# Kernel tuning notes

Hardware: AMD Instinct MI355X
Metric: run time of the kernel (lower is better)

## Reference

```python
import jax, jax.numpy as jnp
import numpy as np
import math

N_BITS = 3
N_EMBD = 2048
N_HEAD = 16
B, T = 1, 2048


def fake_quant_act(x, bits=N_BITS):
    # Brevitas Int8ActPerTensorFloat at 3 bits: signed, non-narrow range [-4, 3]
    qmin, qmax = -(2 ** (bits - 1)), 2 ** (bits - 1) - 1
    s = jax.lax.stop_gradient(jnp.max(jnp.abs(x))) / (2 ** (bits - 1))
    q = jnp.clip(jnp.round(x / s), qmin, qmax) * s
    return x + jax.lax.stop_gradient(q - x)  # STE


def fake_quant_weight(w, bits=N_BITS):
    # Int8WeightPerTensorFloat, narrow_range=True at 3 bits: range [-3, 3]
    qmax = 2 ** (bits - 1) - 1
    s = jax.lax.stop_gradient(jnp.max(jnp.abs(w))) / qmax
    q = jnp.clip(jnp.round(w / s), -qmax, qmax) * s
    return w + jax.lax.stop_gradient(q - w)  # STE


def setup_inputs() -> dict:
    key = jax.random.key(0)
    ks = jax.random.split(key, 7)
    W_STD = 0.02  # GPT-style init keeps exp(att) in range (own_softmax has no max-subtract)
    x = jax.random.normal(ks[0], (B, T, N_EMBD), dtype=jnp.float32)
    W1 = jax.random.normal(ks[1], (N_EMBD, N_EMBD), dtype=jnp.float32) * W_STD
    W2 = jax.random.normal(ks[2], (N_EMBD, N_EMBD), dtype=jnp.float32) * W_STD
    W3 = jax.random.normal(ks[3], (N_EMBD, N_EMBD), dtype=jnp.float32) * W_STD
    b1 = jax.random.normal(ks[4], (N_EMBD,), dtype=jnp.float32) * W_STD
    b2 = jax.random.normal(ks[5], (N_EMBD,), dtype=jnp.float32) * W_STD
    b3 = jax.random.normal(ks[6], (N_EMBD,), dtype=jnp.float32) * W_STD
    return {"x": x, "W1": W1, "b1": b1, "W2": W2, "b2": b2, "W3": W3, "b3": b3}


def reference(x, W1, b1, W2, b2, W3, b3):
    hs = N_EMBD // N_HEAD
    xq = fake_quant_act(x)  # quant_inp
    q = xq @ fake_quant_weight(W1).T + b1  # c_attn1
    k = xq @ fake_quant_weight(W2).T + b2  # c_attn2
    v = xq @ fake_quant_weight(W3).T + b3  # c_attn3
    # [B,T,C] -> [B,nh,T,hs]
    q = q.reshape(B, T, N_HEAD, hs).transpose(0, 2, 1, 3)
    k = k.reshape(B, T, N_HEAD, hs).transpose(0, 2, 1, 3)
    v = v.reshape(B, T, N_HEAD, hs).transpose(0, 2, 1, 3)
    att = jnp.einsum("bhqd,bhkd->bhqk", q, k) * (1.0 / math.sqrt(hs))
    # own_softmax: exp normalized over dim=1 == the HEAD axis (faithful to source; no mask)
    e = jnp.exp(att)
    att = e / jnp.sum(e, axis=1, keepdims=True)
    # attn_dropout p=0 -> identity; c_proj never applied in forward
    y = jnp.einsum("bhqk,bhkd->bhqd", att, v)  # [B,nh,T,hs]
    return y
```

## Files before the change

### kernel.cpp

```cpp
#include <hip/hip_runtime.h>
#include <hip/hip_bf16.h>

typedef short bf16x8 __attribute__((ext_vector_type(8)));
typedef float f32x4 __attribute__((ext_vector_type(4)));
typedef unsigned short u16;

constexpr int TOKS = 2048;
constexpr int EMB  = 2048;
constexpr int NH   = 16;
constexpr int HS   = 128;
constexpr float RSQ = 0.08838834764831845f;

constexpr size_t OFF_SCAL = 0;
constexpr size_t OFF_QX   = 1024;
constexpr size_t SZ_MAT   = (size_t)TOKS * EMB * 2;
constexpr size_t OFF_QW   = OFF_QX + SZ_MAT;
constexpr size_t OFF_Q    = OFF_QW + 3 * SZ_MAT;
constexpr size_t OFF_K    = OFF_Q + SZ_MAT;
constexpr size_t OFF_V    = OFF_K + SZ_MAT;
constexpr size_t OFF_VT   = OFF_V + SZ_MAT;
constexpr size_t OFF_DEN  = OFF_VT + SZ_MAT;

#define VMCNT(n) asm volatile("s_waitcnt vmcnt(" #n ")" ::: "memory")
#define LGKM0()  asm volatile("s_waitcnt lgkmcnt(0)" ::: "memory")
#define BAR()    do { asm volatile("" ::: "memory"); __builtin_amdgcn_s_barrier(); asm volatile("" ::: "memory"); } while (0)

__device__ __forceinline__ u16 f2b(float f) {
  unsigned u = __float_as_uint(f);
  unsigned r = (u + 0x7fffu + ((u >> 16) & 1u)) >> 16;
  return (u16)r;
}

__device__ __forceinline__ unsigned cvtpk(float a, float b) {
  unsigned r;
  asm("v_cvt_pk_bf16_f32 %0, %1, %2" : "=v"(r) : "v"(a), "v"(b));
  return r;
}

__device__ __forceinline__ void gload16(const void* g, void* l) {
  __builtin_amdgcn_global_load_lds(
      (const __attribute__((address_space(1))) unsigned int*)g,
      (__attribute__((address_space(3))) unsigned int*)l, 16, 0, 0);
}

__global__ void k_init(int* scal) {
  if (threadIdx.x < 4) scal[threadIdx.x] = 0;
}

__global__ void k_absmax(const float* __restrict__ x, const float* __restrict__ w1,
                         const float* __restrict__ w2, const float* __restrict__ w3,
                         int* scal) {
  const float* src = (blockIdx.y == 0) ? x : (blockIdx.y == 1) ? w1 : (blockIdx.y == 2) ? w2 : w3;
  const float4* s4 = (const float4*)src;
  int idx = blockIdx.x * 256 + threadIdx.x;
  float m = 0.f;
  for (int i = 0; i < 16; ++i) {
    float4 v = s4[idx + i * 65536];
    m = fmaxf(m, fmaxf(fmaxf(fabsf(v.x), fabsf(v.y)), fmaxf(fabsf(v.z), fabsf(v.w))));
  }
  for (int o = 32; o; o >>= 1) m = fmaxf(m, __shfl_down(m, o));
  __shared__ float red[4];
  if ((threadIdx.x & 63) == 0) red[threadIdx.x >> 6] = m;
  __syncthreads();
  if (threadIdx.x == 0) {
    m = fmaxf(fmaxf(red[0], red[1]), fmaxf(red[2], red[3]));
    atomicMax(&scal[blockIdx.y], __float_as_int(m));
  }
}

__global__ void k_quant(const float* __restrict__ x, const float* __restrict__ w1,
                        const float* __restrict__ w2, const float* __restrict__ w3,
                        u16* qx, u16* qw, const int* scal) {
  int a = blockIdx.y;
  const float* src = (a == 0) ? x : (a == 1) ? w1 : (a == 2) ? w2 : w3;
  u16* dst = (a == 0) ? qx : qw + (size_t)(a - 1) * TOKS * EMB;
  float mx = __int_as_float(scal[a]);
  float s = (a == 0) ? mx * 0.25f : mx / 3.0f;
  float lo = (a == 0) ? -4.f : -3.f;
  const float hi = 3.f;
  int idx = blockIdx.x * 256 + threadIdx.x;
  for (int i = 0; i < 16; ++i) {
    int j = idx + i * 65536;
    float4 v = ((const float4*)src)[j];
    ushort4 o;
    o.x = f2b(fminf(fmaxf(rintf(v.x / s), lo), hi));
    o.y = f2b(fminf(fmaxf(rintf(v.y / s), lo), hi));
    o.z = f2b(fminf(fmaxf(rintf(v.z / s), lo), hi));
    o.w = f2b(fminf(fmaxf(rintf(v.w / s), lo), hi));
    ((ushort4*)dst)[j] = o;
  }
}

__global__ __launch_bounds__(256, 3) void k_gemm(const u16* __restrict__ qx, const u16* __restrict__ qw,
    const float* __restrict__ b1, const float* __restrict__ b2, const float* __restrict__ b3,
    const int* __restrict__ scal, u16* qo, u16* ko, u16* vo) {
  int z = blockIdx.z;
  const u16* W = qw + (size_t)z * TOKS * EMB;
  const float* bias = (z == 0) ? b1 : (z == 1) ? b2 : b3;
  u16* out = (z == 0) ? qo : (z == 1) ? ko : vo;
  float sx = __int_as_float(scal[0]) * 0.25f;
  float sw = __int_as_float(scal[1 + z]) / 3.0f;
  float alpha = sx * sw;
  float extra = (z == 0) ? RSQ : 1.0f;
  int t0 = blockIdx.y * 128, o0 = blockIdx.x * 128;
  __shared__ __align__(16) u16 As[128 * 64];
  __shared__ __align__(16) u16 Bs[128 * 64];
  int tid = threadIdx.x, lane = tid & 63, wid = tid >> 6;
  int mh = (wid >> 1) * 64, nh = (wid & 1) * 64;
  f32x4 acc[4][4] = {};
  const char* Ab = (const char*)qx;
  const char* Bb = (const char*)W;
  for (int kk = 0; kk < 32; ++kk) {
#pragma unroll
    for (int p = 0; p < 4; ++p) {
      int L = p * 4096 + tid * 16;
      int r = L >> 7;
      int s = ((L >> 4) & 7) ^ (r & 7);
      gload16(Ab + (size_t)(t0 + r) * 4096 + kk * 128 + s * 16,
              (char*)As + p * 4096 + wid * 1024);
      gload16(Bb + (size_t)(o0 + r) * 4096 + kk * 128 + s * 16,
              (char*)Bs + p * 4096 + wid * 1024);
    }
    __syncthreads();
#pragma unroll
    for (int ks = 0; ks < 2; ++ks) {
      bf16x8 af[4], bfr[4];
#pragma unroll
      for (int m = 0; m < 4; ++m) {
        int row = mh + m * 16 + (lane & 15);
        int sl = (ks * 4 + (lane >> 4)) ^ (row & 7);
        af[m] = *(const bf16x8*)((const char*)As + row * 128 + sl * 16);
      }
#pragma unroll
      for (int n = 0; n < 4; ++n) {
        int row = nh + n * 16 + (lane & 15);
        int sl = (ks * 4 + (lane >> 4)) ^ (row & 7);
        bfr[n] = *(const bf16x8*)((const char*)Bs + row * 128 + sl * 16);
      }
#pragma unroll
      for (int m = 0; m < 4; ++m)
#pragma unroll
        for (int n = 0; n < 4; ++n)
          acc[m][n] = __builtin_amdgcn_mfma_f32_16x16x32_bf16(af[m], bfr[n], acc[m][n], 0, 0, 0);
    }
    __syncthreads();
  }
#pragma unroll
  for (int m = 0; m < 4; ++m)
#pragma unroll
    for (int n = 0; n < 4; ++n) {
      int ocol = o0 + nh + n * 16 + (lane & 15);
      float bb = bias[ocol];
#pragma unroll
      for (int r = 0; r < 4; ++r) {
        int trow = t0 + mh + m * 16 + (lane >> 4) * 4 + r;
        float v = (acc[m][n][r] * alpha + bb) * extra;
        out[(size_t)trow * EMB + ocol] = f2b(v);
      }
    }
}

__global__ void k_transpose(const u16* __restrict__ v, u16* vt) {
  int h = blockIdx.z, d0 = blockIdx.y * 64, t0 = blockIdx.x * 64;
  __shared__ u16 tile[64][65];
  int tid = threadIdx.x;
  for (int i = 0; i < 16; ++i) {
    int idx = i * 256 + tid, r = idx >> 6, c = idx & 63;
    tile[r][c] = v[(size_t)(t0 + r) * EMB + h * HS + d0 + c];
  }
  __syncthreads();
  for (int i = 0; i < 16; ++i) {
    int idx = i * 256 + tid, r = idx >> 6, c = idx & 63;
    vt[(size_t)(h * HS + d0 + r) * TOKS + t0 + c] = tile[c][r];
  }
}

__global__ __launch_bounds__(256, 3) void k_denom(const u16* __restrict__ q, const u16* __restrict__ k,
                                                  u16* __restrict__ invden) {
  int bid = blockIdx.x;
  int qy = bid & 15, kx = bid >> 4;
  int qt0 = qy * 128, kt0 = kx * 64;
  __shared__ __align__(16) u16 Qs[2][128 * 64];
  __shared__ __align__(16) u16 Ksm[2][64 * 64];
  int tid = threadIdx.x, lane = tid & 63, wid = tid >> 6;
  int wq = (wid >> 1) * 64, wk = (wid & 1) * 32;
  f32x4 acc[4][2] = {}, dd[4][2] = {};
  auto stage = [&](int st, int buf) {
#pragma unroll
    for (int p = 0; p < 4; ++p) {
      int L = p * 4096 + tid * 16;
      int r = L >> 7;
      int s = ((L >> 4) & 7) ^ (r & 7);
      gload16((const char*)q + (size_t)(qt0 + r) * 4096 + st * 128 + s * 16,
              (char*)Qs[buf] + p * 4096 + wid * 1024);
    }
#pragma unroll
    for (int p = 0; p < 2; ++p) {
      int L = p * 4096 + tid * 16;
      int r = L >> 7;
      int s = ((L >> 4) & 7) ^ (r & 7);
      gload16((const char*)k + (size_t)(kt0 + r) * 4096 + st * 128 + s * 16,
              (char*)Ksm[buf] + p * 4096 + wid * 1024);
    }
  };
  stage(0, 0);
  for (int st = 0; st < 32; ++st) {
    int cur = st & 1;
    if (st < 31) { stage(st + 1, cur ^ 1); VMCNT(6); } else { VMCNT(0); }
    BAR();
    __builtin_amdgcn_s_setprio(1);
#pragma unroll
    for (int ks = 0; ks < 2; ++ks) {
      bf16x8 af[4], bfr[2];
#pragma unroll
      for (int m = 0; m < 4; ++m) {
        int row = wq + m * 16 + (lane & 15);
        int sl = (ks * 4 + (lane >> 4)) ^ (row & 7);
        af[m] = *(const bf16x8*)((const char*)Qs[cur] + row * 128 + sl * 16);
      }
#pragma unroll
      for (int n = 0; n < 2; ++n) {
        int row = wk + n * 16 + (lane & 15);
        int sl = (ks * 4 + (lane >> 4)) ^ (row & 7);
        bfr[n] = *(const bf16x8*)((const char*)Ksm[cur] + row * 128 + sl * 16);
      }
#pragma unroll
      for (int m = 0; m < 4; ++m)
#pragma unroll
        for (int n = 0; n < 2; ++n)
          acc[m][n] = __builtin_amdgcn_mfma_f32_16x16x32_bf16(af[m], bfr[n], acc[m][n], 0, 0, 0);
    }
    __builtin_amdgcn_s_setprio(0);
    BAR();
    if (st & 1) {
#pragma unroll
      for (int m = 0; m < 4; ++m)
#pragma unroll
        for (int n = 0; n < 2; ++n) {
#pragma unroll
          for (int r = 0; r < 4; ++r) dd[m][n][r] += __expf(acc[m][n][r]);
          acc[m][n] = f32x4{0.f, 0.f, 0.f, 0.f};
        }
    }
  }
#pragma unroll
  for (int m = 0; m < 4; ++m)
#pragma unroll
    for (int n = 0; n < 2; ++n)
#pragma unroll
      for (int r = 0; r < 4; ++r) {
        int qrow = qt0 + wq + m * 16 + (lane >> 4) * 4 + r;
        int kcol = kt0 + wk + n * 16 + (lane & 15);
        invden[(size_t)qrow * TOKS + kcol] = f2b(1.0f / dd[m][n][r]);
      }
}

__global__ __launch_bounds__(256, 2) void k_attn(const u16* __restrict__ q, const u16* __restrict__ k,
                                                 const u16* __restrict__ vt, const u16* __restrict__ invden,
                                                 float* __restrict__ out) {
  int bid = blockIdx.x;
  int h = (bid & 7) * 2 + ((bid >> 3) & 1);
  int qt0 = (bid >> 4) * 64;
  __shared__ __align__(16) u16 Ks[2][64 * 128];
  __shared__ __align__(16) u16 Vs[2][128 * 64];
  __shared__ __align__(16) u16 Ps[64 * 64];
  int tid = threadIdx.x, lane = tid & 63, wid = tid >> 6;

  auto stageKV = [&](int kb, int buf) {
#pragma unroll
    for (int p = 0; p < 4; ++p) {
      int L = p * 4096 + tid * 16;
      int r = L >> 8;
      int s = ((L >> 4) & 15) ^ (r & 7);
      gload16((const char*)k + (size_t)(kb * 64 + r) * 4096 + h * 256 + s * 16,
              (char*)Ks[buf] + p * 4096 + wid * 1024);
    }
#pragma unroll
    for (int p = 0; p < 4; ++p) {
      int L = p * 4096 + tid * 16;
      int r = L >> 7;
      int s = ((L >> 4) & 7) ^ (r & 7);
      gload16((const char*)vt + (size_t)(h * HS + r) * 4096 + kb * 128 + s * 16,
              (char*)Vs[buf] + p * 4096 + wid * 1024);
    }
  };
  const u16* dinv = invden + (size_t)qt0 * TOKS;
  uint2 dvA[4], dvB[4];

  stageKV(0, 0);
#pragma unroll
  for (int m = 0; m < 4; ++m) {
    int qr = m * 16 + (lane & 15);
    dvA[m] = *(const uint2*)&dinv[(size_t)qr * TOKS + wid * 16 + (lane >> 4) * 4];
  }
  bf16x8 qf[4][4];
#pragma unroll
  for (int m = 0; m < 4; ++m)
#pragma unroll
    for (int c = 0; c < 4; ++c)
      qf[m][c] = *(const bf16x8*)(q + (size_t)(qt0 + m * 16 + (lane & 15)) * EMB
                                  + h * HS + c * 32 + (lane >> 4) * 8);
  f32x4 yacc[4][2] = {};

#define ITER(KB, CUR, DVU, DVP, LAST)                                           \
  {                                                                             \
    if (!(LAST)) {                                                              \
      stageKV((KB) + 1, (CUR) ^ 1);                                             \
      _Pragma("unroll")                                                         \
      for (int m = 0; m < 4; ++m) {                                             \
        int qr = m * 16 + (lane & 15);                                          \
        DVP[m] = *(const uint2*)&dinv[(size_t)qr * TOKS + ((KB) + 1) * 64 +     \
                                      wid * 16 + (lane >> 4) * 4];              \
      }                                                                         \
      VMCNT(12);                                                                \
    } else {                                                                    \
      VMCNT(0);                                                                 \
    }                                                                           \
    BAR();                                                                      \
    f32x4 pacc[4] = {};                                                         \
    __builtin_amdgcn_s_setprio(1);                                              \
    _Pragma("unroll")                                                           \
    for (int c = 0; c < 4; ++c) {                                               \
      int row = wid * 16 + (lane & 15);                                         \
      int sl = (c * 4 + (lane >> 4)) ^ (row & 7);                               \
      bf16x8 bk = *(const bf16x8*)((const char*)Ks[CUR] + row * 256 + sl * 16); \
      _Pragma("unroll")                                                         \
      for (int m = 0; m < 4; ++m)                                               \
        pacc[m] = __builtin_amdgcn_mfma_f32_16x16x32_bf16(bk, qf[m][c], pacc[m], 0, 0, 0); \
    }                                                                           \
    __builtin_amdgcn_s_setprio(0);                                              \
    _Pragma("unroll")                                                           \
    for (int m = 0; m < 4; ++m) {                                               \
      int qr = m * 16 + (lane & 15);                                            \
      float d0 = __uint_as_float(DVU[m].x << 16);                               \
      float d1 = __uint_as_float(DVU[m].x & 0xffff0000u);                       \
      float d2 = __uint_as_float(DVU[m].y << 16);                               \
      float d3 = __uint_as_float(DVU[m].y & 0xffff0000u);                       \
      float e0 = __expf(pacc[m][0]) * d0;                                       \
      float e1 = __expf(pacc[m][1]) * d1;                                       \
      float e2 = __expf(pacc[m][2]) * d2;                                       \
      float e3 = __expf(pacc[m][3]) * d3;                                       \
      uint2 pk;                                                                 \
      pk.x = cvtpk(e0, e1);                                                     \
      pk.y = cvtpk(e2, e3);                                                     \
      int kby = wid * 32 + (lane >> 4) * 8;                                     \
      *(uint2*)((char*)Ps + qr * 128 + (kby ^ ((qr & 7) << 4))) = pk;           \
    }                                                                           \
    LGKM0();                                                                    \
    BAR();                                                                      \
    __builtin_amdgcn_s_setprio(1);                                              \
    _Pragma("unroll")                                                           \
    for (int ks = 0; ks < 2; ++ks) {                                            \
      bf16x8 pa[4], bv[2];                                                      \
      _Pragma("unroll")                                                         \
      for (int m = 0; m < 4; ++m) {                                             \
        int row = m * 16 + (lane & 15);                                         \
        int off = (ks * 64 + (lane >> 4) * 16) ^ ((row & 7) << 4);              \
        pa[m] = *(const bf16x8*)((const char*)Ps + row * 128 + off);            \
      }                                                                         \
      _Pragma("unroll")                                                         \
      for (int j = 0; j < 2; ++j) {                                             \
        int row = wid * 32 + j * 16 + (lane & 15);                              \
        int sl = (ks * 4 + (lane >> 4)) ^ (row & 7);                            \
        bv[j] = *(const bf16x8*)((const char*)Vs[CUR] + row * 128 + sl * 16);   \
      }                                                                         \
      _Pragma("unroll")                                                         \
      for (int m = 0; m < 4; ++m)                                               \
        _Pragma("unroll")                                                       \
        for (int j = 0; j < 2; ++j)                                             \
          yacc[m][j] = __builtin_amdgcn_mfma_f32_16x16x32_bf16(pa[m], bv[j], yacc[m][j], 0, 0, 0); \
    }                                                                           \
    __builtin_amdgcn_s_setprio(0);                                              \
    BAR();                                                                      \
  }

  for (int t = 0; t < 15; ++t) {
    int kbE = 2 * t, kbO = 2 * t + 1;
    ITER(kbE, 0, dvA, dvB, false);
    ITER(kbO, 1, dvB, dvA, false);
  }
  ITER(30, 0, dvA, dvB, false);
  ITER(31, 1, dvB, dvA, true);
#undef ITER

#pragma unroll
  for (int m = 0; m < 4; ++m)
#pragma unroll
    for (int j = 0; j < 2; ++j)
#pragma unroll
      for (int r = 0; r < 4; ++r) {
        int trow = qt0 + m * 16 + (lane >> 4) * 4 + r;
        int dcol = wid * 32 + j * 16 + (lane & 15);
        out[(size_t)(h * TOKS + trow) * HS + dcol] = yacc[m][j][r];
      }
}

extern "C" void kernel_launch(void* const* d_in, const int* in_sizes, int n_in,
                              void* d_out, int out_size, void* d_ws, size_t ws_size,
                              hipStream_t stream) {
  const float* x  = (const float*)d_in[0];
  const float* W1 = (const float*)d_in[1];
  const float* b1 = (const float*)d_in[2];
  const float* W2 = (const float*)d_in[3];
  const float* b2 = (const float*)d_in[4];
  const float* W3 = (const float*)d_in[5];
  const float* b3 = (const float*)d_in[6];
  char* ws = (char*)d_ws;
  int*   scal   = (int*)(ws + OFF_SCAL);
  u16*   qx     = (u16*)(ws + OFF_QX);
  u16*   qw     = (u16*)(ws + OFF_QW);
  u16*   qo     = (u16*)(ws + OFF_Q);
  u16*   ko     = (u16*)(ws + OFF_K);
  u16*   vo     = (u16*)(ws + OFF_V);
  u16*   vt     = (u16*)(ws + OFF_VT);
  u16*   invden = (u16*)(ws + OFF_DEN);
  float* y      = (float*)d_out;

  hipLaunchKernelGGL(k_init, dim3(1), dim3(64), 0, stream, scal);
  hipLaunchKernelGGL(k_absmax, dim3(256, 4), dim3(256), 0, stream, x, W1, W2, W3, scal);
  hipLaunchKernelGGL(k_quant, dim3(256, 4), dim3(256), 0, stream, x, W1, W2, W3, qx, qw, scal);
  hipLaunchKernelGGL(k_gemm, dim3(16, 16, 3), dim3(256), 0, stream,
                     qx, qw, b1, b2, b3, scal, qo, ko, vo);
  hipLaunchKernelGGL(k_transpose, dim3(32, 2, 16), dim3(256), 0, stream, vo, vt);
  hipLaunchKernelGGL(k_denom, dim3(512), dim3(256), 0, stream, qo, ko, invden);
  hipLaunchKernelGGL(k_attn, dim3(512), dim3(256), 0, stream, qo, ko, vt, invden, y);
}
```

Before: 193.3 us.

## Use int8 MFMA for QKV projection and load V directly to registers in attention

The quantized activations and weights are now stored as int8 codes instead of bf16, and the QKV projection uses the i32 16x16x64 int8 MFMA with 64-wide K steps. This halves the operand bytes and the number of K iterations, and the integer results are exact. Separately, the attention kernel stops staging V^T through LDS and loads V fragments straight into registers with prefetch. P is double-buffered in LDS, which removes the trailing barrier per iteration. The risk is extra VGPR pressure from the register-held V prefetch, and uncoalesced global V loads compared with the LDS path.

```diff
diff --git a/kernel.cpp b/kernel.cpp
--- a/kernel.cpp
+++ b/kernel.cpp
@@ -3,6 +3,8 @@
 
 typedef short bf16x8 __attribute__((ext_vector_type(8)));
 typedef float f32x4 __attribute__((ext_vector_type(4)));
+typedef int   i32x4 __attribute__((ext_vector_type(4)));
+typedef unsigned u32x2 __attribute__((ext_vector_type(2)));
 typedef unsigned short u16;
 
 constexpr int TOKS = 2048;
@@ -41,6 +43,17 @@
   __builtin_amdgcn_global_load_lds(
       (const __attribute__((address_space(1))) unsigned int*)g,
       (__attribute__((address_space(3))) unsigned int*)l, 16, 0, 0);
+}
+
+__device__ __forceinline__ bf16x8 gload_dx4(const void* p) {
+  bf16x8 r;
+  asm volatile("global_load_dwordx4 %0, %1, off" : "=v"(r) : "v"(p));
+  return r;
+}
+__device__ __forceinline__ u32x2 gload_dx2(const void* p) {
+  u32x2 r;
+  asm volatile("global_load_dwordx2 %0, %1, off" : "=v"(r) : "v"(p));
+  return r;
 }
 
 __global__ void k_init(int* scal) {
@@ -70,10 +83,10 @@
 
 __global__ void k_quant(const float* __restrict__ x, const float* __restrict__ w1,
                         const float* __restrict__ w2, const float* __restrict__ w3,
-                        u16* qx, u16* qw, const int* scal) {
+                        char* qx, char* qw, const int* scal) {
   int a = blockIdx.y;
   const float* src = (a == 0) ? x : (a == 1) ? w1 : (a == 2) ? w2 : w3;
-  u16* dst = (a == 0) ? qx : qw + (size_t)(a - 1) * TOKS * EMB;
+  char* dst = (a == 0) ? qx : qw + (size_t)(a - 1) * TOKS * EMB;
   float mx = __int_as_float(scal[a]);
   float s = (a == 0) ? mx * 0.25f : mx / 3.0f;
   float lo = (a == 0) ? -4.f : -3.f;
@@ -82,20 +95,21 @@
   for (int i = 0; i < 16; ++i) {
     int j = idx + i * 65536;
     float4 v = ((const float4*)src)[j];
-    ushort4 o;
-    o.x = f2b(fminf(fmaxf(rintf(v.x / s), lo), hi));
-    o.y = f2b(fminf(fmaxf(rintf(v.y / s), lo), hi));
-    o.z = f2b(fminf(fmaxf(rintf(v.z / s), lo), hi));
-    o.w = f2b(fminf(fmaxf(rintf(v.w / s), lo), hi));
-    ((ushort4*)dst)[j] = o;
-  }
-}
-
-__global__ __launch_bounds__(256, 3) void k_gemm(const u16* __restrict__ qx, const u16* __restrict__ qw,
+    int i0 = (int)fminf(fmaxf(rintf(v.x / s), lo), hi);
+    int i1 = (int)fminf(fmaxf(rintf(v.y / s), lo), hi);
+    int i2 = (int)fminf(fmaxf(rintf(v.z / s), lo), hi);
+    int i3 = (int)fminf(fmaxf(rintf(v.w / s), lo), hi);
+    unsigned o = (unsigned)(unsigned char)i0 | ((unsigned)(unsigned char)i1 << 8) |
+                 ((unsigned)(unsigned char)i2 << 16) | ((unsigned)(unsigned char)i3 << 24);
+    ((unsigned*)dst)[j] = o;
+  }
+}
+
+__global__ __launch_bounds__(256, 3) void k_gemm(const char* __restrict__ qx, const char* __restrict__ qw,
     const float* __restrict__ b1, const float* __restrict__ b2, const float* __restrict__ b3,
     const int* __restrict__ scal, u16* qo, u16* ko, u16* vo) {
   int z = blockIdx.z;
-  const u16* W = qw + (size_t)z * TOKS * EMB;
+  const char* W = qw + (size_t)z * TOKS * EMB;
   const float* bias = (z == 0) ? b1 : (z == 1) ? b2 : b3;
   u16* out = (z == 0) ? qo : (z == 1) ? ko : vo;
   float sx = __int_as_float(scal[0]) * 0.25f;
@@ -103,45 +117,43 @@
   float alpha = sx * sw;
   float extra = (z == 0) ? RSQ : 1.0f;
   int t0 = blockIdx.y * 128, o0 = blockIdx.x * 128;
-  __shared__ __align__(16) u16 As[128 * 64];
-  __shared__ __align__(16) u16 Bs[128 * 64];
+  __shared__ __align__(16) char As[128 * 128];
+  __shared__ __align__(16) char Bs[128 * 128];
   int tid = threadIdx.x, lane = tid & 63, wid = tid >> 6;
   int mh = (wid >> 1) * 64, nh = (wid & 1) * 64;
-  f32x4 acc[4][4] = {};
-  const char* Ab = (const char*)qx;
-  const char* Bb = (const char*)W;
-  for (int kk = 0; kk < 32; ++kk) {
+  i32x4 acc[4][4] = {};
+  for (int kk = 0; kk < 16; ++kk) {
 #pragma unroll
     for (int p = 0; p < 4; ++p) {
       int L = p * 4096 + tid * 16;
       int r = L >> 7;
       int s = ((L >> 4) & 7) ^ (r & 7);
-      gload16(Ab + (size_t)(t0 + r) * 4096 + kk * 128 + s * 16,
-              (char*)As + p * 4096 + wid * 1024);
-      gload16(Bb + (size_t)(o0 + r) * 4096 + kk * 128 + s * 16,
-              (char*)Bs + p * 4096 + wid * 1024);
+      gload16(qx + (size_t)(t0 + r) * 2048 + kk * 128 + s * 16,
+              As + p * 4096 + wid * 1024);
+      gload16(W + (size_t)(o0 + r) * 2048 + kk * 128 + s * 16,
+              Bs + p * 4096 + wid * 1024);
     }
     __syncthreads();
 #pragma unroll
     for (int ks = 0; ks < 2; ++ks) {
-      bf16x8 af[4], bfr[4];
+      i32x4 af[4], bfr[4];
 #pragma unroll
       for (int m = 0; m < 4; ++m) {
         int row = mh + m * 16 + (lane & 15);
         int sl = (ks * 4 + (lane >> 4)) ^ (row & 7);
-        af[m] = *(const bf16x8*)((const char*)As + row * 128 + sl * 16);
+        af[m] = *(const i32x4*)(As + row * 128 + sl * 16);
       }
 #pragma unroll
       for (int n = 0; n < 4; ++n) {
         int row = nh + n * 16 + (lane & 15);
         int sl = (ks * 4 + (lane >> 4)) ^ (row & 7);
-        bfr[n] = *(const bf16x8*)((const char*)Bs + row * 128 + sl * 16);
+        bfr[n] = *(const i32x4*)(Bs + row * 128 + sl * 16);
       }
 #pragma unroll
       for (int m = 0; m < 4; ++m)
 #pragma unroll
         for (int n = 0; n < 4; ++n)
-          acc[m][n] = __builtin_amdgcn_mfma_f32_16x16x32_bf16(af[m], bfr[n], acc[m][n], 0, 0, 0);
+          acc[m][n] = __builtin_amdgcn_mfma_i32_16x16x64_i8(af[m], bfr[n], acc[m][n], 0, 0, 0);
     }
     __syncthreads();
   }
@@ -154,7 +166,7 @@
 #pragma unroll
       for (int r = 0; r < 4; ++r) {
         int trow = t0 + mh + m * 16 + (lane >> 4) * 4 + r;
-        float v = (acc[m][n][r] * alpha + bb) * extra;
+        float v = ((float)acc[m][n][r] * alpha + bb) * extra;
         out[(size_t)trow * EMB + ocol] = f2b(v);
       }
     }
@@ -262,11 +274,10 @@
   int h = (bid & 7) * 2 + ((bid >> 3) & 1);
   int qt0 = (bid >> 4) * 64;
   __shared__ __align__(16) u16 Ks[2][64 * 128];
-  __shared__ __align__(16) u16 Vs[2][128 * 64];
-  __shared__ __align__(16) u16 Ps[64 * 64];
+  __shared__ __align__(16) u16 Ps[2][64 * 64];
   int tid = threadIdx.x, lane = tid & 63, wid = tid >> 6;
 
-  auto stageKV = [&](int kb, int buf) {
+  auto stageK = [&](int kb, int buf) {
 #pragma unroll
     for (int p = 0; p < 4; ++p) {
       int L = p * 4096 + tid * 16;
@@ -275,24 +286,23 @@
       gload16((const char*)k + (size_t)(kb * 64 + r) * 4096 + h * 256 + s * 16,
               (char*)Ks[buf] + p * 4096 + wid * 1024);
     }
-#pragma unroll
-    for (int p = 0; p < 4; ++p) {
-      int L = p * 4096 + tid * 16;
-      int r = L >> 7;
-      int s = ((L >> 4) & 7) ^ (r & 7);
-      gload16((const char*)vt + (size_t)(h * HS + r) * 4096 + kb * 128 + s * 16,
-              (char*)Vs[buf] + p * 4096 + wid * 1024);
-    }
   };
-  const u16* dinv = invden + (size_t)qt0 * TOKS;
-  uint2 dvA[4], dvB[4];
-
-  stageKV(0, 0);
-#pragma unroll
-  for (int m = 0; m < 4; ++m) {
-    int qr = m * 16 + (lane & 15);
-    dvA[m] = *(const uint2*)&dinv[(size_t)qr * TOKS + wid * 16 + (lane >> 4) * 4];
-  }
+  const u16* vbase = vt + ((size_t)(h * HS + wid * 32 + (lane & 15))) * TOKS + (lane >> 4) * 8;
+  const u16* dvbase = invden + ((size_t)(qt0 + (lane & 15))) * TOKS + wid * 16 + (lane >> 4) * 4;
+
+  bf16x8 vA[4], vB[4];
+  u32x2 dvA[4], dvB[4];
+
+  stageK(0, 0);
+#pragma unroll
+  for (int j = 0; j < 2; ++j)
+#pragma unroll
+    for (int ks = 0; ks < 2; ++ks)
+      vA[j * 2 + ks] = gload_dx4(vbase + (size_t)j * 16 * TOKS + ks * 32);
+#pragma unroll
+  for (int m = 0; m < 4; ++m)
+    dvA[m] = gload_dx2(dvbase + (size_t)m * 16 * TOKS);
+
   bf16x8 qf[4][4];
 #pragma unroll
   for (int m = 0; m < 4; ++m)
@@ -302,20 +312,24 @@
                                   + h * HS + c * 32 + (lane >> 4) * 8);
   f32x4 yacc[4][2] = {};
 
-#define ITER(KB, CUR, DVU, DVP, LAST)                                           \
+#define ITER(KB, CUR, VU, VP, DVU, DVP, LAST)                                   \
   {                                                                             \
     if (!(LAST)) {                                                              \
-      stageKV((KB) + 1, (CUR) ^ 1);                                             \
+      stageK((KB) + 1, (CUR) ^ 1);                                              \
       _Pragma("unroll")                                                         \
-      for (int m = 0; m < 4; ++m) {                                             \
-        int qr = m * 16 + (lane & 15);                                          \
-        DVP[m] = *(const uint2*)&dinv[(size_t)qr * TOKS + ((KB) + 1) * 64 +     \
-                                      wid * 16 + (lane >> 4) * 4];              \
-      }                                                                         \
+      for (int j = 0; j < 2; ++j)                                               \
+        _Pragma("unroll")                                                       \
+        for (int ks = 0; ks < 2; ++ks)                                          \
+          VP[j * 2 + ks] = gload_dx4(vbase + (size_t)j * 16 * TOKS +            \
+                                     ((KB) + 1) * 64 + ks * 32);                \
+      _Pragma("unroll")                                                         \
+      for (int m = 0; m < 4; ++m)                                               \
+        DVP[m] = gload_dx2(dvbase + (size_t)m * 16 * TOKS + ((KB) + 1) * 64);   \
       VMCNT(12);                                                                \
     } else {                                                                    \
       VMCNT(0);                                                                 \
     }                                                                           \
+    __builtin_amdgcn_sched_barrier(0);                                          \
     BAR();                                                                      \
     f32x4 pacc[4] = {};                                                         \
     __builtin_amdgcn_s_setprio(1);                                              \
@@ -332,10 +346,10 @@
     _Pragma("unroll")                                                           \
     for (int m = 0; m < 4; ++m) {                                               \
       int qr = m * 16 + (lane & 15);                                            \
-      float d0 = __uint_as_float(DVU[m].x << 16);                               \
-      float d1 = __uint_as_float(DVU[m].x & 0xffff0000u);                       \
-      float d2 = __uint_as_float(DVU[m].y << 16);                               \
-      float d3 = __uint_as_float(DVU[m].y & 0xffff0000u);                       \
+      float d0 = __uint_as_float(DVU[m][0] << 16);                              \
+      float d1 = __uint_as_float(DVU[m][0] & 0xffff0000u);                      \
+      float d2 = __uint_as_float(DVU[m][1] << 16);                              \
+      float d3 = __uint_as_float(DVU[m][1] & 0xffff0000u);                      \
       float e0 = __expf(pacc[m][0]) * d0;                                       \
       float e1 = __expf(pacc[m][1]) * d1;                                       \
       float e2 = __expf(pacc[m][2]) * d2;                                       \
@@ -344,43 +358,36 @@
       pk.x = cvtpk(e0, e1);                                                     \
       pk.y = cvtpk(e2, e3);                                                     \
       int kby = wid * 32 + (lane >> 4) * 8;                                     \
-      *(uint2*)((char*)Ps + qr * 128 + (kby ^ ((qr & 7) << 4))) = pk;           \
+      *(uint2*)((char*)Ps[CUR] + qr * 128 + (kby ^ ((qr & 7) << 4))) = pk;      \
     }                                                                           \
     LGKM0();                                                                    \
     BAR();                                                                      \
+    __builtin_amdgcn_sched_barrier(0);                                          \
     __builtin_amdgcn_s_setprio(1);                                              \
     _Pragma("unroll")                                                           \
     for (int ks = 0; ks < 2; ++ks) {                                            \
-      bf16x8 pa[4], bv[2];                                                      \
+      bf16x8 pa[4];                                                             \
       _Pragma("unroll")                                                         \
       for (int m = 0; m < 4; ++m) {                                             \
         int row = m * 16 + (lane & 15);                                         \
         int off = (ks * 64 + (lane >> 4) * 16) ^ ((row & 7) << 4);              \
-        pa[m] = *(const bf16x8*)((const char*)Ps + row * 128 + off);            \
-      }                                                                         \
-      _Pragma("unroll")                                                         \
-      for (int j = 0; j < 2; ++j) {                                             \
-        int row = wid * 32 + j * 16 + (lane & 15);                              \
-        int sl = (ks * 4 + (lane >> 4)) ^ (row & 7);                            \
-        bv[j] = *(const bf16x8*)((const char*)Vs[CUR] + row * 128 + sl * 16);   \
+        pa[m] = *(const bf16x8*)((const char*)Ps[CUR] + row * 128 + off);       \
       }                                                                         \
       _Pragma("unroll")                                                         \
       for (int m = 0; m < 4; ++m)                                               \
         _Pragma("unroll")                                                       \
         for (int j = 0; j < 2; ++j)                                             \
-          yacc[m][j] = __builtin_amdgcn_mfma_f32_16x16x32_bf16(pa[m], bv[j], yacc[m][j], 0, 0, 0); \
+          yacc[m][j] = __builtin_amdgcn_mfma_f32_16x16x32_bf16(pa[m], VU[j * 2 + ks], yacc[m][j], 0, 0, 0); \
     }                                                                           \
     __builtin_amdgcn_s_setprio(0);                                              \
-    BAR();                                                                      \
   }
 
   for (int t = 0; t < 15; ++t) {
-    int kbE = 2 * t, kbO = 2 * t + 1;
-    ITER(kbE, 0, dvA, dvB, false);
-    ITER(kbO, 1, dvB, dvA, false);
-  }
-  ITER(30, 0, dvA, dvB, false);
-  ITER(31, 1, dvB, dvA, true);
+    ITER(2 * t, 0, vA, vB, dvA, dvB, false);
+    ITER(2 * t + 1, 1, vB, vA, dvB, dvA, false);
+  }
+  ITER(30, 0, vA, vB, dvA, dvB, false);
+  ITER(31, 1, vB, vA, dvB, dvA, true);
 #undef ITER
 
 #pragma unroll
@@ -407,8 +414,8 @@
   const float* b3 = (const float*)d_in[6];
   char* ws = (char*)d_ws;
   int*   scal   = (int*)(ws + OFF_SCAL);
-  u16*   qx     = (u16*)(ws + OFF_QX);
-  u16*   qw     = (u16*)(ws + OFF_QW);
+  char*  qx8    = (char*)(ws + OFF_QX);
+  char*  qw8    = (char*)(ws + OFF_QW);
   u16*   qo     = (u16*)(ws + OFF_Q);
   u16*   ko     = (u16*)(ws + OFF_K);
   u16*   vo     = (u16*)(ws + OFF_V);
@@ -418,9 +425,9 @@
 
   hipLaunchKernelGGL(k_init, dim3(1), dim3(64), 0, stream, scal);
   hipLaunchKernelGGL(k_absmax, dim3(256, 4), dim3(256), 0, stream, x, W1, W2, W3, scal);
-  hipLaunchKernelGGL(k_quant, dim3(256, 4), dim3(256), 0, stream, x, W1, W2, W3, qx, qw, scal);
+  hipLaunchKernelGGL(k_quant, dim3(256, 4), dim3(256), 0, stream, x, W1, W2, W3, qx8, qw8, scal);
   hipLaunchKernelGGL(k_gemm, dim3(16, 16, 3), dim3(256), 0, stream,
-                     qx, qw, b1, b2, b3, scal, qo, ko, vo);
+                     qx8, qw8, b1, b2, b3, scal, qo, ko, vo);
   hipLaunchKernelGGL(k_transpose, dim3(32, 2, 16), dim3(256), 0, stream, vo, vt);
   hipLaunchKernelGGL(k_denom, dim3(512), dim3(256), 0, stream, qo, ko, invden);
   hipLaunchKernelGGL(k_attn, dim3(512), dim3(256), 0, stream, qo, ko, vt, invden, y);
```

After: 176.3 us. 8.8% less time.
